# Kernel tuning notes

Hardware: AMD Instinct MI355X
Metric: run time of the kernel (lower is better)

## Reference

```python
import jax, jax.numpy as jnp
import numpy as np
from jax import lax

B, C, H, W = 8, 384, 32, 32
HEADS, GROUPS = 12, 3
CG = C // GROUPS          # 128 channels per offset group
HD = C // HEADS           # 32 head dim
NS = H * W                # sampled kv points (one per query location)
EPS = 1e-5


def setup_inputs() -> dict:
    key = jax.random.key(0)
    ks = jax.random.split(key, 10)
    w = lambda k, sh, sc=0.02: (jax.random.normal(k, sh, jnp.float32) * sc)
    return {
        "x1": jax.random.normal(ks[0], (B, C, H, W), jnp.float32),
        "x2": jax.random.normal(ks[1], (B, C, H, W), jnp.float32),
        "Wq": w(ks[2], (C, C)), "bq": jnp.zeros((C,), jnp.float32),
        "Wk": w(ks[3], (C, C)), "bk": jnp.zeros((C,), jnp.float32),
        "Wv": w(ks[4], (C, C)), "bv": jnp.zeros((C,), jnp.float32),
        "Wo": w(ks[5], (C, C)), "bo": jnp.zeros((C,), jnp.float32),
        "off_dw": w(ks[6], (CG, 1, 5, 5)),       # depthwise 5x5 offset conv
        "off_dw_b": jnp.zeros((CG,), jnp.float32),
        "ln_g": jnp.ones((CG,), jnp.float32),
        "ln_b": jnp.zeros((CG,), jnp.float32),
        "off_w": w(ks[7], (2, CG), 0.01),         # 1x1 conv -> 2 offset channels
    }


def _conv1x1(x, Wm, bm):
    return jnp.einsum('oc,bchw->bohw', Wm, x) + bm[None, :, None, None]


def _ref_grid():
    # normalized reference points in [-1,1], channel 0 = x (width), 1 = y (height)
    xs = (jnp.arange(W, dtype=jnp.float32) + 0.5) / W * 2.0 - 1.0
    ys = (jnp.arange(H, dtype=jnp.float32) + 0.5) / H * 2.0 - 1.0
    gy, gx = jnp.meshgrid(ys, xs, indexing='ij')   # [H,W]
    return jnp.stack([gx, gy], axis=0)             # [2,H,W]


def _forward(x1, x2, Wq, bq, Wk, bk, Wv, bv, Wo, bo,
             off_dw, off_dw_b, ln_g, ln_b, off_w):
    BG = B * GROUPS
    q = _conv1x1(x1, Wq, bq)                                   # [B,C,H,W]

    # --- offset network (per group) ---
    qg = q.reshape(BG, CG, H, W)
    t = lax.conv_general_dilated(qg, off_dw, (1, 1), 'SAME',
                                 dimension_numbers=('NCHW', 'OIHW', 'NCHW'),
                                 feature_group_count=CG)
    t = t + off_dw_b[None, :, None, None]
    mu = jnp.mean(t, axis=1, keepdims=True)
    var = jnp.var(t, axis=1, keepdims=True)
    t = (t - mu) * lax.rsqrt(var + EPS)
    t = t * ln_g[None, :, None, None] + ln_b[None, :, None, None]
    t = jax.nn.gelu(t)
    off = jnp.einsum('oc,bchw->bohw', off_w, t)                # [BG,2,H,W]

    pos = jnp.clip(off + _ref_grid()[None], -1.0, 1.0)         # [BG,2,H,W]
    px = pos[:, 0].reshape(BG, NS)
    py = pos[:, 1].reshape(BG, NS)

    # --- bilinear grid_sample of x2 (align_corners=True) ---
    ix = (px + 1.0) * 0.5 * (W - 1)
    iy = (py + 1.0) * 0.5 * (H - 1)
    x0f, y0f = jnp.floor(ix), jnp.floor(iy)
    wx, wy = ix - x0f, iy - y0f
    x0 = jnp.clip(x0f.astype(jnp.int32), 0, W - 1)
    x1i = jnp.clip(x0 + 1, 0, W - 1)
    y0 = jnp.clip(y0f.astype(jnp.int32), 0, H - 1)
    y1i = jnp.clip(y0 + 1, 0, H - 1)

    x2g = x2.reshape(BG, CG, H * W)

    def gather(yi, xi):
        idx = yi * W + xi                                      # [BG,NS]
        idx = jnp.broadcast_to(idx[:, None, :], (BG, CG, NS))
        return jnp.take_along_axis(x2g, idx, axis=2)           # [BG,CG,NS]

    v00, v01 = gather(y0, x0), gather(y0, x1i)
    v10, v11 = gather(y1i, x0), gather(y1i, x1i)
    wx_, wy_ = wx[:, None, :], wy[:, None, :]
    samp = (v00 * (1 - wx_) * (1 - wy_) + v01 * wx_ * (1 - wy_)
            + v10 * (1 - wx_) * wy_ + v11 * wx_ * wy_)         # [BG,CG,NS]
    samp = samp.reshape(B, C, NS)

    # --- multi-head attention between q and sampled k/v ---
    k = jnp.einsum('oc,bcn->bon', Wk, samp) + bk[None, :, None]
    v = jnp.einsum('oc,bcn->bon', Wv, samp) + bv[None, :, None]
    qf = q.reshape(B, HEADS, HD, NS)
    kf = k.reshape(B, HEADS, HD, NS)
    vf = v.reshape(B, HEADS, HD, NS)
    scale = 1.0 / np.sqrt(HD).astype(np.float32)
    attn = jax.nn.softmax(jnp.einsum('bhdq,bhdk->bhqk', qf * scale, kf), axis=-1)
    out = jnp.einsum('bhqk,bhdk->bhdq', attn, vf).reshape(B, C, H, W)
    y = _conv1x1(out, Wo, bo)
    return x1 + y                                              # residual add (drop_path=0 -> Identity)


def reference(x1, x2, Wq, bq, Wk, bk, Wv, bv, Wo, bo,
              off_dw, off_dw_b, ln_g, ln_b, off_w):
    return _forward(x1, x2, Wq, bq, Wk, bk, Wv, bv, Wo, bo,
                    off_dw, off_dw_b, ln_g, ln_b, off_w)
```

## Files before the change

### kernel.cpp

```cpp
#include <hip/hip_runtime.h>
#include <math.h>

#define B_  8
#define C_  384
#define NS_ 1024
#define HEADS_ 12
#define HD_ 32
#define GROUPS_ 3
#define CG_ 128
#define EPS_ 1e-5f
#define QSC2 (0.17677669529663687f * 1.4426950408889634f)

typedef __attribute__((ext_vector_type(8))) short bf16x8;
typedef __attribute__((ext_vector_type(4))) short bf16x4;
typedef __attribute__((ext_vector_type(4))) float f32x4;
typedef __attribute__((ext_vector_type(8))) __bf16 b8;

static __device__ __forceinline__ short f2b(float f) {
  union { float f; unsigned u; } v; v.f = f;
  unsigned r = v.u + 0x7fffu + ((v.u >> 16) & 1u);
  return (short)(r >> 16);
}
static __device__ __forceinline__ float b2f(short s) {
  union { unsigned u; float f; } v; v.u = ((unsigned)(unsigned short)s) << 16;
  return v.f;
}

#if __has_builtin(__builtin_amdgcn_exp2f)
#define EXP2(x) __builtin_amdgcn_exp2f(x)
#else
#define EXP2(x) exp2f(x)
#endif

static __device__ __forceinline__ unsigned cvtpk(float lo, float hi) {
  unsigned r;
  asm("v_cvt_pk_bf16_f32 %0, %1, %2" : "=v"(r) : "v"(lo), "v"(hi));
  return r;
}

static __device__ __forceinline__ f32x4 MFMA(bf16x8 a, bf16x8 b, f32x4 c) {
  return __builtin_amdgcn_mfma_f32_16x16x32_bf16(
      __builtin_bit_cast(b8, a), __builtin_bit_cast(b8, b), c, 0, 0, 0);
}

__global__ void convw(const float* __restrict__ s0, const float* __restrict__ s1,
                      const float* __restrict__ s2, const float* __restrict__ s3,
                      short* __restrict__ d0, short* __restrict__ d1,
                      short* __restrict__ d2, short* __restrict__ d3, int n) {
  int i = blockIdx.x * 256 + threadIdx.x;
  if (i >= n) return;
  const float* s = blockIdx.y == 0 ? s0 : blockIdx.y == 1 ? s1 : blockIdx.y == 2 ? s2 : s3;
  short*       d = blockIdx.y == 0 ? d0 : blockIdx.y == 1 ? d1 : blockIdx.y == 2 ? d2 : d3;
  d[i] = f2b(s[i]);
}

__global__ __launch_bounds__(256) void transp(const float* __restrict__ src,
                                              short* __restrict__ dst) {
  __shared__ float tl[32][33];
  int n0 = blockIdx.x * 32, c0 = blockIdx.y * 32, b = blockIdx.z;
  int tx = threadIdx.x & 31, ty = threadIdx.x >> 5;
#pragma unroll
  for (int i = 0; i < 4; ++i)
    tl[ty + 8 * i][tx] = src[((size_t)b * C_ + c0 + ty + 8 * i) * NS_ + n0 + tx];
  __syncthreads();
#pragma unroll
  for (int i = 0; i < 4; ++i)
    dst[((size_t)b * NS_ + n0 + ty + 8 * i) * C_ + c0 + tx] = f2b(tl[tx][ty + 8 * i]);
}

#define GLOADA(kc_, AF)                                                        \
  _Pragma("unroll")                                                            \
  for (int rt = 0; rt < 4; ++rt)                                               \
    AF[rt] = *(const bf16x8*)(Ab + (size_t)(n0 + wr + rt * 16 + r15) * C_ +    \
                              (kc_) + g * 8);
#define GLOADB(kc_, BF, WP, MOFF)                                              \
  _Pragma("unroll")                                                            \
  for (int ct = 0; ct < 4; ++ct)                                               \
    BF[ct] = *(const bf16x8*)((WP) + (size_t)((MOFF) + ct * 16 + r15) * C_ +   \
                              (kc_) + g * 8);
#define GMFMA(AF, BF)                                                          \
  _Pragma("unroll")                                                            \
  for (int rt = 0; rt < 4; ++rt)                                               \
    _Pragma("unroll")                                                          \
    for (int ct = 0; ct < 4; ++ct) acc[rt][ct] = MFMA(AF[rt], BF[ct], acc[rt][ct]);

template <int MODE>
__global__ __launch_bounds__(256) void gemm_nm(
    const short* __restrict__ A, const short* __restrict__ Wb,
    const float* __restrict__ bias, const float* __restrict__ res,
    short* __restrict__ outb, float* __restrict__ outf) {
  int b = blockIdx.z;
  int n0 = blockIdx.x * 128;
  int m0 = blockIdx.y * 128;
  int wv = threadIdx.x >> 6;
  int lane = threadIdx.x & 63;
  int g = lane >> 4, r15 = lane & 15;
  int wr = (wv >> 1) * 64, wc = (wv & 1) * 64;

  const short* Ab = A + (size_t)b * NS_ * C_;
  f32x4 acc[4][4];
#pragma unroll
  for (int i = 0; i < 4; ++i)
#pragma unroll
    for (int j = 0; j < 4; ++j) acc[i][j] = (f32x4){0.f, 0.f, 0.f, 0.f};

  bf16x8 afA[4], bfA[4], afB[4], bfB[4];
  GLOADA(0, afA); GLOADB(0, bfA, Wb, m0 + wc);
#pragma unroll
  for (int cp = 0; cp < 6; ++cp) {
    GLOADA(64 * cp + 32, afB); GLOADB(64 * cp + 32, bfB, Wb, m0 + wc);
    GMFMA(afA, bfA);
    if (cp < 5) { GLOADA(64 * cp + 64, afA); GLOADB(64 * cp + 64, bfA, Wb, m0 + wc); }
    GMFMA(afB, bfB);
  }

#pragma unroll
  for (int rt = 0; rt < 4; ++rt)
#pragma unroll
    for (int ct = 0; ct < 4; ++ct) {
      int m = m0 + wc + ct * 16 + r15;
      int nb = n0 + wr + rt * 16 + g * 4;
      float bv = bias[m];
      f32x4 v = acc[rt][ct];
      v.x += bv; v.y += bv; v.z += bv; v.w += bv;
      if (MODE == 1) {
        *(f32x4*)(outf + ((size_t)b * C_ + m) * NS_ + nb) = v;
        outb[((size_t)b * NS_ + nb + 0) * C_ + m] = f2b(v.x * QSC2);
        outb[((size_t)b * NS_ + nb + 1) * C_ + m] = f2b(v.y * QSC2);
        outb[((size_t)b * NS_ + nb + 2) * C_ + m] = f2b(v.z * QSC2);
        outb[((size_t)b * NS_ + nb + 3) * C_ + m] = f2b(v.w * QSC2);
      } else {
        const f32x4 rv = *(const f32x4*)(res + ((size_t)b * C_ + m) * NS_ + nb);
        v.x += rv.x; v.y += rv.y; v.z += rv.z; v.w += rv.w;
        *(f32x4*)(outf + ((size_t)b * C_ + m) * NS_ + nb) = v;
      }
    }
}

__global__ __launch_bounds__(256) void gemm_kv(
    const short* __restrict__ A, const short* __restrict__ Wkb,
    const short* __restrict__ Wvb, const float* __restrict__ bkv,
    const float* __restrict__ bvv, short* __restrict__ kblk,
    short* __restrict__ vblk) {
  int b = blockIdx.z;
  int n0 = blockIdx.x * 128;
  int m0 = blockIdx.y * 64;
  int wv = threadIdx.x >> 6;
  int lane = threadIdx.x & 63;
  int g = lane >> 4, r15 = lane & 15;
  int wr = (wv >> 1) * 64;
  int isv = wv & 1;
  const short* Wsel = isv ? Wvb : Wkb;
  const float* bsel = isv ? bvv : bkv;

  const short* Ab = A + (size_t)b * NS_ * C_;
  f32x4 acc[4][4];
#pragma unroll
  for (int i = 0; i < 4; ++i)
#pragma unroll
    for (int j = 0; j < 4; ++j) acc[i][j] = (f32x4){0.f, 0.f, 0.f, 0.f};

  bf16x8 afA[4], bfA[4], afB[4], bfB[4];
  GLOADA(0, afA); GLOADB(0, bfA, Wsel, m0);
#pragma unroll
  for (int cp = 0; cp < 6; ++cp) {
    GLOADA(64 * cp + 32, afB); GLOADB(64 * cp + 32, bfB, Wsel, m0);
    GMFMA(afA, bfA);
    if (cp < 5) { GLOADA(64 * cp + 64, afA); GLOADB(64 * cp + 64, bfA, Wsel, m0); }
    GMFMA(afB, bfB);
  }

#pragma unroll
  for (int rt = 0; rt < 4; ++rt)
#pragma unroll
    for (int ct = 0; ct < 4; ++ct) {
      int m = m0 + ct * 16 + r15;
      int nb = n0 + wr + rt * 16 + g * 4;
      float bv = bsel[m];
      f32x4 v = acc[rt][ct];
      v.x += bv; v.y += bv; v.z += bv; v.w += bv;
      int h = m >> 5, dh = m & 31;
      if (!isv) {
        size_t hb = ((size_t)(b * HEADS_ + h) * 32 + (nb >> 5)) * 1024 +
                    (((nb >> 4) & 1) ? 512 : 0);
        int base_l = (nb & 15) | ((dh >> 3) << 4);
        int jj = dh & 7;
        kblk[hb + (size_t)(base_l + 0) * 8 + jj] = f2b(v.x);
        kblk[hb + (size_t)(base_l + 1) * 8 + jj] = f2b(v.y);
        kblk[hb + (size_t)(base_l + 2) * 8 + jj] = f2b(v.z);
        kblk[hb + (size_t)(base_l + 3) * 8 + jj] = f2b(v.w);
      } else {
        int dt = dh >> 4, q15v = dh & 15;
        int kk = nb & 31;
        int half = kk >> 4, gk = (kk & 15) >> 2;
        size_t off = ((size_t)(b * HEADS_ + h) * 32 + (nb >> 5)) * 1024 +
                     dt * 512 + (size_t)((q15v | (gk << 4))) * 8 + half * 4;
        bf16x4 s4 = {f2b(v.x), f2b(v.y), f2b(v.z), f2b(v.w)};
        *(bf16x4*)(vblk + off) = s4;
      }
    }
}

__global__ __launch_bounds__(256) void offsample3(
    const float* __restrict__ qd, const float* __restrict__ x2,
    const float* __restrict__ dw, const float* __restrict__ dwb,
    const float* __restrict__ lng, const float* __restrict__ lnb,
    const float* __restrict__ offw, short* __restrict__ samp) {
  __shared__ float redS[4][16], redSS[4][16], redO0[4][16], redO1[4][16];
  int bg = blockIdx.x, t16 = blockIdx.y;
  int tid = threadIdx.x;
  int cc = tid >> 4, p = tid & 15;
  int wv = tid >> 6, lane = tid & 63;
  int n = t16 * 16 + p;
  int y = t16 >> 1;
  int x = ((t16 & 1) << 4) + p;
  int c0 = cc << 3;

  const float* qb = qd + (size_t)bg * CG_ * NS_;

  float a[8];
  float s = 0.f, ss = 0.f;
#pragma unroll
  for (int i = 0; i < 8; ++i) {
    int c = c0 + i;
    const float* qc = qb + (size_t)c * NS_;
    const float* wc = dw + c * 25;
    float acc = dwb[c];
#pragma unroll
    for (int dy = -2; dy <= 2; ++dy) {
      int yy = y + dy;
      if (yy < 0 || yy > 31) continue;
      const float* row = qc + yy * 32;
      const float* wr_ = wc + (dy + 2) * 5;
#pragma unroll
      for (int dx = -2; dx <= 2; ++dx) {
        int xx = x + dx;
        int xcl = min(max(xx, 0), 31);
        float v = row[xcl];
        if (xx != xcl) v = 0.f;
        acc = fmaf(v, wr_[dx + 2], acc);
      }
    }
    a[i] = acc;
    s += acc; ss += acc * acc;
  }

  s  += __shfl_xor(s, 16);  s  += __shfl_xor(s, 32);
  ss += __shfl_xor(ss, 16); ss += __shfl_xor(ss, 32);
  if (lane < 16) { redS[wv][lane] = s; redSS[wv][lane] = ss; }
  __syncthreads();
  float S  = (redS[0][p]  + redS[1][p])  + (redS[2][p]  + redS[3][p]);
  float SS = (redSS[0][p] + redSS[1][p]) + (redSS[2][p] + redSS[3][p]);
  float mu = S * (1.f / CG_);
  float var = SS * (1.f / CG_) - mu * mu;
  float rs = rsqrtf(var + EPS_);

  float o0 = 0.f, o1 = 0.f;
#pragma unroll
  for (int i = 0; i < 8; ++i) {
    int c = c0 + i;
    float z = (a[i] - mu) * rs * lng[c] + lnb[c];
    float u = z * fmaf(0.044715f * z, z, 1.f);
    float e = __expf(-1.5957691216057308f * u);
    float ge = z * __builtin_amdgcn_rcpf(1.f + e);
    o0 = fmaf(offw[c], ge, o0);
    o1 = fmaf(offw[CG_ + c], ge, o1);
  }
  o0 += __shfl_xor(o0, 16); o0 += __shfl_xor(o0, 32);
  o1 += __shfl_xor(o1, 16); o1 += __shfl_xor(o1, 32);
  if (lane < 16) { redO0[wv][lane] = o0; redO1[wv][lane] = o1; }
  __syncthreads();
  float off0 = (redO0[0][p] + redO0[1][p]) + (redO0[2][p] + redO0[3][p]);
  float off1 = (redO1[0][p] + redO1[1][p]) + (redO1[2][p] + redO1[3][p]);

  float gx = (x + 0.5f) * 0.0625f - 1.f;
  float gy = (y + 0.5f) * 0.0625f - 1.f;
  float px = fminf(fmaxf(off0 + gx, -1.f), 1.f);
  float py = fminf(fmaxf(off1 + gy, -1.f), 1.f);
  float ix = (px + 1.f) * 0.5f * 31.f;
  float iy = (py + 1.f) * 0.5f * 31.f;
  float x0f = floorf(ix), y0f = floorf(iy);
  float wx = ix - x0f, wy = iy - y0f;
  int x0 = min(max((int)x0f, 0), 31), x1i = min(x0 + 1, 31);
  int y0 = min(max((int)y0f, 0), 31), y1i = min(y0 + 1, 31);
  int i00 = y0 * 32 + x0,  i01 = y0 * 32 + x1i;
  int i10 = y1i * 32 + x0, i11 = y1i * 32 + x1i;
  float w00 = (1.f - wx) * (1.f - wy), w01 = wx * (1.f - wy);
  float w10 = (1.f - wx) * wy,         w11 = wx * wy;

  int b = bg / GROUPS_, gi = bg % GROUPS_;
  const float* xb = x2 + (size_t)bg * CG_ * NS_;
  short out8[8];
#pragma unroll
  for (int i = 0; i < 8; ++i) {
    const float* xc = xb + (size_t)(c0 + i) * NS_;
    float v = w00 * xc[i00] + w01 * xc[i01] + w10 * xc[i10] + w11 * xc[i11];
    out8[i] = f2b(v);
  }
  *(bf16x8*)(samp + ((size_t)b * NS_ + n) * C_ + gi * CG_ + c0) = *(bf16x8*)out8;
}

__global__ __launch_bounds__(256) void attn_blk(
    const short* __restrict__ qn, const short* __restrict__ kblk,
    const short* __restrict__ vblk, short* __restrict__ op0,
    short* __restrict__ op1, float* __restrict__ lp) {
  int L = blockIdx.x;
  int tq = L >> 3;
  int task = (L & 7) + ((tq % 24) << 3);
  int qblk = tq / 24;
  int bh = task >> 1, s = task & 1;
  int b = bh / HEADS_, h = bh % HEADS_;
  int wv = threadIdx.x >> 6, lane = threadIdx.x & 63;
  int g = lane >> 4, q15 = lane & 15;
  int q0 = qblk * 128 + wv * 32;

  const short* Qb = qn + (size_t)b * NS_ * C_ + h * HD_;
  const short* Kc = kblk + ((size_t)(b * HEADS_ + h) * 32 + s * 16) * 1024 + lane * 8;
  const short* Vc = vblk + ((size_t)(b * HEADS_ + h) * 32 + s * 16) * 1024 + lane * 8;

  bf16x8 qf[2];
  qf[0] = *(const bf16x8*)(Qb + (size_t)(q0 + q15) * C_ + g * 8);
  qf[1] = *(const bf16x8*)(Qb + (size_t)(q0 + 16 + q15) * C_ + g * 8);

  f32x4 o[2][2];
  o[0][0] = o[0][1] = o[1][0] = o[1][1] = (f32x4){0.f, 0.f, 0.f, 0.f};
  f32x4 lv[2];
  lv[0] = lv[1] = (f32x4){0.f, 0.f, 0.f, 0.f};

#define LOADC(c_, K0, K1, V0, V1)                                              \
  {                                                                            \
    K0 = *(const bf16x8*)(Kc + (c_) * 1024);                                   \
    K1 = *(const bf16x8*)(Kc + (c_) * 1024 + 512);                             \
    V0 = *(const bf16x8*)(Vc + (c_) * 1024);                                   \
    V1 = *(const bf16x8*)(Vc + (c_) * 1024 + 512);                             \
  }

#define COMPUTEC(K0, K1, V0, V1)                                               \
  {                                                                            \
    _Pragma("unroll")                                                          \
    for (int qt = 0; qt < 2; ++qt) {                                           \
      f32x4 z_ = {0.f, 0.f, 0.f, 0.f};                                         \
      f32x4 t0 = MFMA(K0, qf[qt], z_);                                         \
      f32x4 t1 = MFMA(K1, qf[qt], z_);                                         \
      f32x4 e0, e1;                                                            \
      e0.x = EXP2(t0.x); e0.y = EXP2(t0.y); e0.z = EXP2(t0.z); e0.w = EXP2(t0.w);\
      e1.x = EXP2(t1.x); e1.y = EXP2(t1.y); e1.z = EXP2(t1.z); e1.w = EXP2(t1.w);\
      lv[qt] += e0; lv[qt] += e1;                                              \
      union { unsigned u[4]; bf16x8 v; } pu;                                   \
      pu.u[0] = cvtpk(e0.x, e0.y);                                             \
      pu.u[1] = cvtpk(e0.z, e0.w);                                             \
      pu.u[2] = cvtpk(e1.x, e1.y);                                             \
      pu.u[3] = cvtpk(e1.z, e1.w);                                             \
      o[qt][0] = MFMA(V0, pu.v, o[qt][0]);                                     \
      o[qt][1] = MFMA(V1, pu.v, o[qt][1]);                                     \
    }                                                                          \
  }

  bf16x8 kA0, kA1, vA0, vA1, kB0, kB1, vB0, vB1;
  LOADC(0, kA0, kA1, vA0, vA1);
#pragma unroll
  for (int cp = 0; cp < 8; ++cp) {
    LOADC(2 * cp + 1, kB0, kB1, vB0, vB1);
    COMPUTEC(kA0, kA1, vA0, vA1);
    if (cp < 7) LOADC(2 * cp + 2, kA0, kA1, vA0, vA1);
    COMPUTEC(kB0, kB1, vB0, vB1);
  }
#undef LOADC
#undef COMPUTEC

  short* opS = s ? op1 : op0;
#pragma unroll
  for (int qt = 0; qt < 2; ++qt) {
    float lt = (lv[qt].x + lv[qt].y) + (lv[qt].z + lv[qt].w);
    lt += __shfl_xor(lt, 16);
    lt += __shfl_xor(lt, 32);
    int q = q0 + qt * 16 + q15;
    if (g == 0) lp[((size_t)(s * B_ + b) * HEADS_ + h) * NS_ + q] = lt;
#pragma unroll
    for (int dt = 0; dt < 2; ++dt) {
      f32x4 ov = o[qt][dt];
      bf16x4 s4 = {f2b(ov.x), f2b(ov.y), f2b(ov.z), f2b(ov.w)};
      *(bf16x4*)(opS + ((size_t)b * NS_ + q) * C_ + h * HD_ + dt * 16 + g * 4) = s4;
    }
  }
}

__global__ __launch_bounds__(256) void attn_merge(
    const short* __restrict__ op0, const short* __restrict__ op1,
    const float* __restrict__ lp, short* __restrict__ on) {
  int idx = blockIdx.x * 256 + threadIdx.x;
  int c8 = idx % (C_ / 8);
  int q  = (idx / (C_ / 8)) % NS_;
  int b  = idx / ((C_ / 8) * NS_);
  int c0 = c8 * 8, h = c0 >> 5;
  size_t off = ((size_t)b * NS_ + q) * C_ + c0;
  bf16x8 a  = *(const bf16x8*)(op0 + off);
  bf16x8 bb = *(const bf16x8*)(op1 + off);
  float l = lp[((size_t)b * HEADS_ + h) * NS_ + q] +
            lp[((size_t)(B_ + b) * HEADS_ + h) * NS_ + q];
  float rl = 1.f / l;
  short r[8];
#pragma unroll
  for (int j = 0; j < 8; ++j) r[j] = f2b((b2f(a[j]) + b2f(bb[j])) * rl);
  *(bf16x8*)(on + off) = *(bf16x8*)r;
}

extern "C" void kernel_launch(void* const* d_in, const int* in_sizes, int n_in,
                              void* d_out, int out_size, void* d_ws, size_t ws_size,
                              hipStream_t stream) {
  const float* x1      = (const float*)d_in[0];
  const float* x2      = (const float*)d_in[1];
  const float* Wq      = (const float*)d_in[2];
  const float* bq      = (const float*)d_in[3];
  const float* Wk      = (const float*)d_in[4];
  const float* bk      = (const float*)d_in[5];
  const float* Wv      = (const float*)d_in[6];
  const float* bv      = (const float*)d_in[7];
  const float* Wo      = (const float*)d_in[8];
  const float* bo      = (const float*)d_in[9];
  const float* off_dw  = (const float*)d_in[10];
  const float* off_dwb = (const float*)d_in[11];
  const float* ln_g    = (const float*)d_in[12];
  const float* ln_b    = (const float*)d_in[13];
  const float* off_w   = (const float*)d_in[14];

  char* base = (char*)d_ws;
  const size_t SZ = (size_t)B_ * C_ * NS_;
  float* q_dC  = (float*)base;
  short* q_nC  = (short*)(base + SZ * 4);
  short* samp  = (short*)(base + SZ * 6);
  short* k_blk = (short*)(base + SZ * 8);
  short* v_blk = (short*)(base + SZ * 10);
  short* o_nC  = (short*)(base + SZ * 12);
  short* x1t   = (short*)(base + SZ * 14);
  short* Wqb   = (short*)(base + SZ * 16);
  short* Wkb   = Wqb + C_ * C_;
  short* Wvb   = Wkb + C_ * C_;
  short* Wob   = Wvb + C_ * C_;
  short* op0   = samp;
  short* op1   = x1t;
  float* lp    = q_dC;

  dim3 gg(NS_ / 128, C_ / 128, B_);

  convw<<<dim3((C_ * C_ + 255) / 256, 4), 256, 0, stream>>>(
      Wq, Wk, Wv, Wo, Wqb, Wkb, Wvb, Wob, C_ * C_);
  transp<<<dim3(NS_ / 32, C_ / 32, B_), 256, 0, stream>>>(x1, x1t);
  gemm_nm<1><<<gg, 256, 0, stream>>>(x1t, Wqb, bq, nullptr, q_nC, q_dC);
  offsample3<<<dim3(B_ * GROUPS_, 64), 256, 0, stream>>>(
      q_dC, x2, off_dw, off_dwb, ln_g, ln_b, off_w, samp);
  gemm_kv<<<dim3(NS_ / 128, C_ / 64, B_), 256, 0, stream>>>(
      samp, Wkb, Wvb, bk, bv, k_blk, v_blk);
  attn_blk<<<dim3(1536), 256, 0, stream>>>(q_nC, k_blk, v_blk, op0, op1, lp);
  attn_merge<<<dim3(B_ * NS_ * (C_ / 8) / 256), 256, 0, stream>>>(op0, op1, lp, o_nC);
  gemm_nm<3><<<gg, 256, 0, stream>>>(o_nC, Wob, bo, x1, nullptr, (float*)d_out);
}
```

Before: 136.2 us.

## Restructure offset sampler with register-tiled depthwise conv and channel-last bf16 x2

Rewrites the offset/sampling kernel so each thread computes a 4-channel by 4-pixel tile of the depthwise 5x5 conv with vectorized row loads. The filter weights are pre-transposed to tap-major order, and the LayerNorm and offset reductions run entirely in wave shuffles, with no shared memory or block barriers. x2 is transposed to channel-last bf16 by an extra kernel, so each bilinear gather reads contiguous 4-channel vectors instead of strided fp32 scalars. This adds two extra kernel launches, a full pass over x2, and bf16 rounding of x2 before interpolation.

```diff
diff --git a/kernel.cpp b/kernel.cpp
--- a/kernel.cpp
+++ b/kernel.cpp
@@ -54,6 +54,15 @@
   d[i] = f2b(s[i]);
 }
 
+__global__ void convdw(const float* __restrict__ dw, float* __restrict__ dwp) {
+  int i = blockIdx.x * 256 + threadIdx.x;
+  if (i < 25 * CG_) {
+    int t = i / CG_, c = i % CG_;
+    dwp[i] = dw[c * 25 + t];
+  }
+}
+
+template <int CH>
 __global__ __launch_bounds__(256) void transp(const float* __restrict__ src,
                                               short* __restrict__ dst) {
   __shared__ float tl[32][33];
@@ -61,11 +70,11 @@
   int tx = threadIdx.x & 31, ty = threadIdx.x >> 5;
 #pragma unroll
   for (int i = 0; i < 4; ++i)
-    tl[ty + 8 * i][tx] = src[((size_t)b * C_ + c0 + ty + 8 * i) * NS_ + n0 + tx];
+    tl[ty + 8 * i][tx] = src[((size_t)b * CH + c0 + ty + 8 * i) * NS_ + n0 + tx];
   __syncthreads();
 #pragma unroll
   for (int i = 0; i < 4; ++i)
-    dst[((size_t)b * NS_ + n0 + ty + 8 * i) * C_ + c0 + tx] = f2b(tl[tx][ty + 8 * i]);
+    dst[((size_t)b * NS_ + n0 + ty + 8 * i) * CH + c0 + tx] = f2b(tl[tx][ty + 8 * i]);
 }
 
 #define GLOADA(kc_, AF)                                                        \
@@ -201,103 +210,133 @@
     }
 }
 
-__global__ __launch_bounds__(256) void offsample3(
-    const float* __restrict__ qd, const float* __restrict__ x2,
-    const float* __restrict__ dw, const float* __restrict__ dwb,
+__global__ __launch_bounds__(256) void offsample4(
+    const float* __restrict__ qd,
+    const short* __restrict__ x2t,
+    const float* __restrict__ dwp,
+    const float* __restrict__ dwb,
     const float* __restrict__ lng, const float* __restrict__ lnb,
     const float* __restrict__ offw, short* __restrict__ samp) {
-  __shared__ float redS[4][16], redSS[4][16], redO0[4][16], redO1[4][16];
-  int bg = blockIdx.x, t16 = blockIdx.y;
+  int bg = blockIdx.x, y = blockIdx.y;
   int tid = threadIdx.x;
-  int cc = tid >> 4, p = tid & 15;
-  int wv = tid >> 6, lane = tid & 63;
-  int n = t16 * 16 + p;
-  int y = t16 >> 1;
-  int x = ((t16 & 1) << 4) + p;
-  int c0 = cc << 3;
-
-  const float* qb = qd + (size_t)bg * CG_ * NS_;
-
-  float a[8];
-  float s = 0.f, ss = 0.f;
-#pragma unroll
-  for (int i = 0; i < 8; ++i) {
-    int c = c0 + i;
-    const float* qc = qb + (size_t)c * NS_;
-    const float* wc = dw + c * 25;
-    float acc = dwb[c];
-#pragma unroll
-    for (int dy = -2; dy <= 2; ++dy) {
-      int yy = y + dy;
-      if (yy < 0 || yy > 31) continue;
-      const float* row = qc + yy * 32;
-      const float* wr_ = wc + (dy + 2) * 5;
-#pragma unroll
-      for (int dx = -2; dx <= 2; ++dx) {
-        int xx = x + dx;
-        int xcl = min(max(xx, 0), 31);
-        float v = row[xcl];
-        if (xx != xcl) v = 0.f;
-        acc = fmaf(v, wr_[dx + 2], acc);
-      }
-    }
-    a[i] = acc;
-    s += acc; ss += acc * acc;
-  }
-
-  s  += __shfl_xor(s, 16);  s  += __shfl_xor(s, 32);
-  ss += __shfl_xor(ss, 16); ss += __shfl_xor(ss, 32);
-  if (lane < 16) { redS[wv][lane] = s; redSS[wv][lane] = ss; }
-  __syncthreads();
-  float S  = (redS[0][p]  + redS[1][p])  + (redS[2][p]  + redS[3][p]);
-  float SS = (redSS[0][p] + redSS[1][p]) + (redSS[2][p] + redSS[3][p]);
-  float mu = S * (1.f / CG_);
-  float var = SS * (1.f / CG_) - mu * mu;
-  float rs = rsqrtf(var + EPS_);
-
-  float o0 = 0.f, o1 = 0.f;
-#pragma unroll
-  for (int i = 0; i < 8; ++i) {
-    int c = c0 + i;
-    float z = (a[i] - mu) * rs * lng[c] + lnb[c];
-    float u = z * fmaf(0.044715f * z, z, 1.f);
-    float e = __expf(-1.5957691216057308f * u);
-    float ge = z * __builtin_amdgcn_rcpf(1.f + e);
-    o0 = fmaf(offw[c], ge, o0);
-    o1 = fmaf(offw[CG_ + c], ge, o1);
-  }
-  o0 += __shfl_xor(o0, 16); o0 += __shfl_xor(o0, 32);
-  o1 += __shfl_xor(o1, 16); o1 += __shfl_xor(o1, 32);
-  if (lane < 16) { redO0[wv][lane] = o0; redO1[wv][lane] = o1; }
-  __syncthreads();
-  float off0 = (redO0[0][p] + redO0[1][p]) + (redO0[2][p] + redO0[3][p]);
-  float off1 = (redO1[0][p] + redO1[1][p]) + (redO1[2][p] + redO1[3][p]);
-
-  float gx = (x + 0.5f) * 0.0625f - 1.f;
+  int xg = tid >> 5, cc = tid & 31;
+  int x0 = xg << 2, c0 = cc << 2;
+
+  const float* qb = qd + ((size_t)bg * CG_ + c0) * NS_;
+
+  f32x4 dwb4 = *(const f32x4*)(dwb + c0);
+  float a[4][4];
+#pragma unroll
+  for (int i = 0; i < 4; ++i)
+#pragma unroll
+    for (int p = 0; p < 4; ++p) a[i][p] = dwb4[i];
+
+#pragma unroll
+  for (int dy = -2; dy <= 2; ++dy) {
+    int yy = y + dy;
+    if (yy < 0 || yy > 31) continue;
+    f32x4 w0 = *(const f32x4*)(dwp + ((dy + 2) * 5 + 0) * CG_ + c0);
+    f32x4 w1 = *(const f32x4*)(dwp + ((dy + 2) * 5 + 1) * CG_ + c0);
+    f32x4 w2 = *(const f32x4*)(dwp + ((dy + 2) * 5 + 2) * CG_ + c0);
+    f32x4 w3 = *(const f32x4*)(dwp + ((dy + 2) * 5 + 3) * CG_ + c0);
+    f32x4 w4 = *(const f32x4*)(dwp + ((dy + 2) * 5 + 4) * CG_ + c0);
+#pragma unroll
+    for (int i = 0; i < 4; ++i) {
+      const float* row = qb + (size_t)i * NS_ + yy * 32;
+      f32x4 wa = (f32x4){0.f, 0.f, 0.f, 0.f};
+      f32x4 wcv = (f32x4){0.f, 0.f, 0.f, 0.f};
+      if (x0 >= 4)  wa  = *(const f32x4*)(row + x0 - 4);
+      f32x4 wb = *(const f32x4*)(row + x0);
+      if (x0 <= 24) wcv = *(const f32x4*)(row + x0 + 4);
+      float w[12] = {wa[0], wa[1], wa[2], wa[3], wb[0], wb[1], wb[2], wb[3],
+                     wcv[0], wcv[1], wcv[2], wcv[3]};
+      float wt[5] = {w0[i], w1[i], w2[i], w3[i], w4[i]};
+#pragma unroll
+      for (int p = 0; p < 4; ++p)
+#pragma unroll
+        for (int j = 0; j < 5; ++j)
+          a[i][p] = fmaf(w[p + j + 2], wt[j], a[i][p]);
+    }
+  }
+
+  f32x4 sum = (f32x4){0.f, 0.f, 0.f, 0.f}, sumsq = sum;
+#pragma unroll
+  for (int i = 0; i < 4; ++i)
+#pragma unroll
+    for (int p = 0; p < 4; ++p) { sum[p] += a[i][p]; sumsq[p] += a[i][p] * a[i][p]; }
+#pragma unroll
+  for (int m = 1; m <= 16; m <<= 1) {
+#pragma unroll
+    for (int p = 0; p < 4; ++p) {
+      sum[p]   += __shfl_xor(sum[p], m);
+      sumsq[p] += __shfl_xor(sumsq[p], m);
+    }
+  }
+  f32x4 mu, rs;
+#pragma unroll
+  for (int p = 0; p < 4; ++p) {
+    mu[p] = sum[p] * (1.f / CG_);
+    float var = sumsq[p] * (1.f / CG_) - mu[p] * mu[p];
+    rs[p] = rsqrtf(var + EPS_);
+  }
+
+  f32x4 lg = *(const f32x4*)(lng + c0);
+  f32x4 lb = *(const f32x4*)(lnb + c0);
+  f32x4 ow0 = *(const f32x4*)(offw + c0);
+  f32x4 ow1 = *(const f32x4*)(offw + CG_ + c0);
+  f32x4 o0 = (f32x4){0.f, 0.f, 0.f, 0.f}, o1 = o0;
+#pragma unroll
+  for (int i = 0; i < 4; ++i)
+#pragma unroll
+    for (int p = 0; p < 4; ++p) {
+      float z = (a[i][p] - mu[p]) * rs[p] * lg[i] + lb[i];
+      float u = z * fmaf(0.044715f * z, z, 1.f);
+      float e = __expf(-1.5957691216057308f * u);
+      float ge = z * __builtin_amdgcn_rcpf(1.f + e);
+      o0[p] = fmaf(ow0[i], ge, o0[p]);
+      o1[p] = fmaf(ow1[i], ge, o1[p]);
+    }
+#pragma unroll
+  for (int m = 1; m <= 16; m <<= 1) {
+#pragma unroll
+    for (int p = 0; p < 4; ++p) {
+      o0[p] += __shfl_xor(o0[p], m);
+      o1[p] += __shfl_xor(o1[p], m);
+    }
+  }
+
+  int b = bg / GROUPS_, gi = bg % GROUPS_;
+  const short* xb = x2t + (size_t)bg * NS_ * CG_ + c0;
   float gy = (y + 0.5f) * 0.0625f - 1.f;
-  float px = fminf(fmaxf(off0 + gx, -1.f), 1.f);
-  float py = fminf(fmaxf(off1 + gy, -1.f), 1.f);
-  float ix = (px + 1.f) * 0.5f * 31.f;
-  float iy = (py + 1.f) * 0.5f * 31.f;
-  float x0f = floorf(ix), y0f = floorf(iy);
-  float wx = ix - x0f, wy = iy - y0f;
-  int x0 = min(max((int)x0f, 0), 31), x1i = min(x0 + 1, 31);
-  int y0 = min(max((int)y0f, 0), 31), y1i = min(y0 + 1, 31);
-  int i00 = y0 * 32 + x0,  i01 = y0 * 32 + x1i;
-  int i10 = y1i * 32 + x0, i11 = y1i * 32 + x1i;
-  float w00 = (1.f - wx) * (1.f - wy), w01 = wx * (1.f - wy);
-  float w10 = (1.f - wx) * wy,         w11 = wx * wy;
-
-  int b = bg / GROUPS_, gi = bg % GROUPS_;
-  const float* xb = x2 + (size_t)bg * CG_ * NS_;
-  short out8[8];
-#pragma unroll
-  for (int i = 0; i < 8; ++i) {
-    const float* xc = xb + (size_t)(c0 + i) * NS_;
-    float v = w00 * xc[i00] + w01 * xc[i01] + w10 * xc[i10] + w11 * xc[i11];
-    out8[i] = f2b(v);
-  }
-  *(bf16x8*)(samp + ((size_t)b * NS_ + n) * C_ + gi * CG_ + c0) = *(bf16x8*)out8;
+#pragma unroll
+  for (int p = 0; p < 4; ++p) {
+    int x = x0 + p, n = y * 32 + x;
+    float gx = (x + 0.5f) * 0.0625f - 1.f;
+    float px = fminf(fmaxf(o0[p] + gx, -1.f), 1.f);
+    float py = fminf(fmaxf(o1[p] + gy, -1.f), 1.f);
+    float ix = (px + 1.f) * 0.5f * 31.f;
+    float iy = (py + 1.f) * 0.5f * 31.f;
+    float x0f = floorf(ix), y0f = floorf(iy);
+    float wx = ix - x0f, wy = iy - y0f;
+    int xa = min(max((int)x0f, 0), 31), xbb = min(xa + 1, 31);
+    int ya = min(max((int)y0f, 0), 31), yb = min(ya + 1, 31);
+    int i00 = ya * 32 + xa, i01 = ya * 32 + xbb;
+    int i10 = yb * 32 + xa, i11 = yb * 32 + xbb;
+    float w00 = (1.f - wx) * (1.f - wy), w01 = wx * (1.f - wy);
+    float w10 = (1.f - wx) * wy,         w11 = wx * wy;
+    bf16x4 v00 = *(const bf16x4*)(xb + (size_t)i00 * CG_);
+    bf16x4 v01 = *(const bf16x4*)(xb + (size_t)i01 * CG_);
+    bf16x4 v10 = *(const bf16x4*)(xb + (size_t)i10 * CG_);
+    bf16x4 v11 = *(const bf16x4*)(xb + (size_t)i11 * CG_);
+    short out4[4];
+#pragma unroll
+    for (int j = 0; j < 4; ++j) {
+      float v = w00 * b2f(v00[j]) + w01 * b2f(v01[j]) +
+                w10 * b2f(v10[j]) + w11 * b2f(v11[j]);
+      out4[j] = f2b(v);
+    }
+    *(bf16x4*)(samp + ((size_t)b * NS_ + n) * C_ + gi * CG_ + c0) = *(bf16x4*)out4;
+  }
 }
 
 __global__ __launch_bounds__(256) void attn_blk(
@@ -437,6 +476,8 @@
   short* Wkb   = Wqb + C_ * C_;
   short* Wvb   = Wkb + C_ * C_;
   short* Wob   = Wvb + C_ * C_;
+  short* x2t   = (short*)(base + SZ * 18);
+  float* dwp   = (float*)(base + SZ * 20);
   short* op0   = samp;
   short* op1   = x1t;
   float* lp    = q_dC;
@@ -445,10 +486,12 @@
 
   convw<<<dim3((C_ * C_ + 255) / 256, 4), 256, 0, stream>>>(
       Wq, Wk, Wv, Wo, Wqb, Wkb, Wvb, Wob, C_ * C_);
-  transp<<<dim3(NS_ / 32, C_ / 32, B_), 256, 0, stream>>>(x1, x1t);
+  convdw<<<dim3(13), 256, 0, stream>>>(off_dw, dwp);
+  transp<C_><<<dim3(NS_ / 32, C_ / 32, B_), 256, 0, stream>>>(x1, x1t);
+  transp<CG_><<<dim3(NS_ / 32, CG_ / 32, B_ * GROUPS_), 256, 0, stream>>>(x2, x2t);
   gemm_nm<1><<<gg, 256, 0, stream>>>(x1t, Wqb, bq, nullptr, q_nC, q_dC);
-  offsample3<<<dim3(B_ * GROUPS_, 64), 256, 0, stream>>>(
-      q_dC, x2, off_dw, off_dwb, ln_g, ln_b, off_w, samp);
+  offsample4<<<dim3(B_ * GROUPS_, 32), 256, 0, stream>>>(
+      q_dC, x2t, dwp, off_dwb, ln_g, ln_b, off_w, samp);
   gemm_kv<<<dim3(NS_ / 128, C_ / 64, B_), 256, 0, stream>>>(
       samp, Wkb, Wvb, bk, bv, k_blk, v_blk);
   attn_blk<<<dim3(1536), 256, 0, stream>>>(q_nC, k_blk, v_blk, op0, op1, lp);
```

Result: slower. 139.8 us (+2.6%).
